# Optimization experiments

Hardware: AMD Instinct MI355X
Metric: run time of the kernel (lower is better)

## Reference

```python
import jax, jax.numpy as jnp
import numpy as np
from jax import lax

R = 3                      # blob_r
S = 2 * R + 1              # 7: maxpool / neighborhood kernel size
THRESH = 0.997
PS_XY = 0.1                # vs_xy
PS_Z = 0.02                # vs_z
ZMIN = -2.0                # zrange[0]
K_PEAKS = 131072           # static upper bound replacing torch.nonzero

_offs = np.arange(S)
_gz, _gy, _gx = np.meshgrid(_offs, _offs, _offs, indexing='ij')  # patch axis order [z,y,x]
GZ = jnp.asarray(_gz.ravel(), dtype=jnp.int32)
GY = jnp.asarray(_gy.ravel(), dtype=jnp.int32)
GX = jnp.asarray(_gx.ravel(), dtype=jnp.int32)
# centroid filters: offsets -r..r along the matching patch axis (matches torch meshgrid layout)
FZ = jnp.asarray((_gz.ravel() - R).astype(np.float32))
FY = jnp.asarray((_gy.ravel() - R).astype(np.float32))
FX = jnp.asarray((_gx.ravel() - R).astype(np.float32))


def setup_inputs() -> dict:
    key = jax.random.key(0)
    pred_vol = jax.random.uniform(key, (1, 1, 128, 512, 512), dtype=jnp.float32)
    return {"pred_vol": pred_vol, "max_peaks": K_PEAKS}


def _forward(pred_vol, max_peaks):
    vol = pred_vol[0, 0]                               # [D,H,W]
    D, H, W = vol.shape
    thr = jnp.where(vol > THRESH, vol, 0.0)
    # MaxPool3d(kernel=2r+1, stride=1, padding=r) == SAME max window (pad with -inf)
    mp = lax.reduce_window(thr, -jnp.inf, lax.max, (S, S, S), (1, 1, 1), [(R, R)] * 3)
    conf = jnp.where((mp > 0.0) & (mp == thr), mp, 0.0)  # local maxima above threshold
    # fixed-size peak extraction (replaces torch.nonzero); zero-valued entries are padding
    vals, idx = lax.top_k(conf.reshape(-1), max_peaks)   # [K], [K]
    z = idx // (H * W)
    y = (idx % (H * W)) // W
    x = idx % W
    padv = jnp.pad(vol, R)                               # ConstantPad3d(r, 0)
    # gather (2r+1)^3 neighborhoods around each peak: [K, S^3]
    patches = padv[z[:, None] + GZ[None, :], y[:, None] + GY[None, :], x[:, None] + GX[None, :]]
    s0 = patches.sum(axis=1)                             # conv3d with ones filter == conf_rec sum
    xloc = jnp.einsum('kp,p->k', patches, FX) / s0
    yloc = jnp.einsum('kp,p->k', patches, FY) / s0
    zloc = jnp.einsum('kp,p->k', patches, FZ) / s0
    xf = x.astype(jnp.float32)
    yf = y.astype(jnp.float32)
    zf = z.astype(jnp.float32)
    xrec = (xf + xloc - (W - 1) / 2.0) * PS_XY
    yrec = (yf + yloc - (H - 1) / 2.0) * PS_XY
    zrec = (zf + zloc + 0.5) * PS_Z + ZMIN
    valid = vals > 0.0
    xyz = jnp.where(valid[:, None], jnp.stack((xrec, yrec, zrec), axis=1), 0.0)  # [K,3]
    out = jnp.concatenate([xyz, vals[:, None]], axis=1)  # [K,4] = (x,y,z,conf), padded rows are 0
    return out, valid


def reference(pred_vol, max_peaks):
    return _forward(pred_vol, max_peaks)
```

## Files before the change

### kernel.cpp

```cpp
#include <hip/hip_runtime.h>

#define DD 128
#define HH 512
#define WW 512
#define NVOX (DD*HH*WW)
#define THRESHV 0.997f
#define KPEAKS 131072
#define PEAK_CAP (1u<<18)
#define NBINS 65536


__global__ void k_init(unsigned* counters, unsigned* hist) {
    unsigned t = blockIdx.x * 1024u + threadIdx.x;
    if (t < 64) counters[t] = 0u;
    if (t < NBINS) hist[t] = 0u;
}

__global__ __launch_bounds__(512, 8)
void k_find(const float4* __restrict__ vol4, const float* __restrict__ vol,
            unsigned* counters, unsigned* hist,
            unsigned long long* keys, float4* psums) {
    __shared__ float4 tile[2048];
    __shared__ unsigned lcnt, pcnt, lbase;
    __shared__ unsigned cidx[384];
    __shared__ unsigned long long lbuf[192];
    __shared__ float4 sbuf[192];
    if (threadIdx.x == 0) { lcnt = 0; pcnt = 0; }
    __syncthreads();

    unsigned t = threadIdx.x;
    unsigned lane = t & 63u;
    unsigned w = t >> 6;
    unsigned blockBase4 = blockIdx.x * 2048u;

#pragma unroll
    for (unsigned i = 0; i < 4; i++) {
        unsigned f = i * 512u + w * 64u;
        const float4* gp = vol4 + blockBase4 + f + lane;
        __builtin_amdgcn_global_load_lds(
            (const __attribute__((address_space(1))) unsigned int*)gp,
            (__attribute__((address_space(3))) unsigned int*)(tile + f),
            16, 0, 0);
    }
    __builtin_amdgcn_s_waitcnt(0);
    __syncthreads();

    unsigned m = 0u;
    float4 v[4];
#pragma unroll
    for (unsigned i = 0; i < 4; i++) v[i] = tile[i * 512u + t];
#pragma unroll
    for (unsigned i = 0; i < 4; i++) {
        m |= (v[i].x > THRESHV ? 1u : 0u) << (4 * i);
        m |= (v[i].y > THRESHV ? 1u : 0u) << (4 * i + 1);
        m |= (v[i].z > THRESHV ? 1u : 0u) << (4 * i + 2);
        m |= (v[i].w > THRESHV ? 1u : 0u) << (4 * i + 3);
    }
    while (m) {
        int b = __ffs(m) - 1;
        m &= m - 1u;
        unsigned f4 = blockBase4 + (unsigned)(b >> 2) * 512u + t;
        cidx[atomicAdd(&lcnt, 1u) & 383u] = f4 * 4u + (unsigned)(b & 3);
    }
    __syncthreads();

    unsigned n = lcnt > 384u ? 384u : lcnt;
    int dz = (int)lane / 7, dy = (int)lane - dz * 7;
    for (unsigned base = w * 2u; base < n; base += 16u) {
        bool has2 = (base + 1u < n);
        unsigned idxA = cidx[base];
        unsigned idxB = has2 ? cidx[base + 1u] : idxA;
        int zA = idxA >> 18, yA = (idxA >> 9) & 511, xA = idxA & 511;
        int zB = idxB >> 18, yB = (idxB >> 9) & 511, xB = idxB & 511;
        int nzA = zA + dz - 3, nyA = yA + dy - 3;
        int nzB = zB + dz - 3, nyB = yB + dy - 3;
        bool rowokA = (lane < 49) && ((unsigned)nzA < DD) && ((unsigned)nyA < HH);
        bool rowokB = (lane < 49) && ((unsigned)nzB < DD) && ((unsigned)nyB < HH);
        size_t rbA = rowokA ? (((size_t)(unsigned)nzA << 18) | ((size_t)(unsigned)nyA << 9))
                            : (((size_t)zA << 18) | ((size_t)yA << 9));
        size_t rbB = rowokB ? (((size_t)(unsigned)nzB << 18) | ((size_t)(unsigned)nyB << 9))
                            : (((size_t)zB << 18) | ((size_t)yB << 9));
        float rvA[7], rvB[7];
        bool intAB = (xA >= 3) && (xA <= WW - 4) && (xB >= 3) && (xB <= WW - 4);
        if (intAB) {
            float4 fA0 = *(const float4*)(vol + rbA + (unsigned)(xA - 3));
            float4 fA1 = *(const float4*)(vol + rbA + (unsigned)(xA + 1));
            float4 fB0 = *(const float4*)(vol + rbB + (unsigned)(xB - 3));
            float4 fB1 = *(const float4*)(vol + rbB + (unsigned)(xB + 1));
            rvA[0] = fA0.x; rvA[1] = fA0.y; rvA[2] = fA0.z; rvA[3] = fA0.w;
            rvA[4] = fA1.x; rvA[5] = fA1.y; rvA[6] = fA1.z;
            rvB[0] = fB0.x; rvB[1] = fB0.y; rvB[2] = fB0.z; rvB[3] = fB0.w;
            rvB[4] = fB1.x; rvB[5] = fB1.y; rvB[6] = fB1.z;
        } else {
#pragma unroll
            for (int d = 0; d < 7; d++) {
                int nxA = xA + d - 3;
                bool okA = (unsigned)nxA < WW;
                float va = vol[rbA + (unsigned)(okA ? nxA : xA)];
                rvA[d] = okA ? va : 0.f;
                int nxB = xB + d - 3;
                bool okB = (unsigned)nxB < WW;
                float vb = vol[rbB + (unsigned)(okB ? nxB : xB)];
                rvB[d] = okB ? vb : 0.f;
            }
        }
        if (!rowokA) {
#pragma unroll
            for (int d = 0; d < 7; d++) rvA[d] = 0.f;
        }
        if (!rowokB) {
#pragma unroll
            for (int d = 0; d < 7; d++) rvB[d] = 0.f;
        }
        float centerA = __shfl(rvA[3], 24);
        float centerB = __shfl(rvB[3], 24);

        {
            bool kill = false;
            float s0r = 0.f, sxr = 0.f;
#pragma unroll
            for (int d = 0; d < 7; d++) {
                kill |= rvA[d] > centerA;
                s0r += rvA[d];
                sxr += rvA[d] * (float)(d - 3);
            }
            if (!__any(kill)) {
                float s0 = s0r, sx = sxr;
                float sy = s0r * (float)(dy - 3);
                float sz = s0r * (float)(dz - 3);
                for (int off = 32; off; off >>= 1) {
                    s0 += __shfl_down(s0, off);
                    sx += __shfl_down(sx, off);
                    sy += __shfl_down(sy, off);
                    sz += __shfl_down(sz, off);
                }
                if (lane == 0) {
                    unsigned bits = __float_as_uint(centerA);
                    atomicAdd(&hist[(~bits) & 0xFFFFu], 1u);
                    unsigned li = atomicAdd(&pcnt, 1u);
                    if (li < 192u) {
                        lbuf[li] = ((unsigned long long)bits << 32) | idxA;
                        sbuf[li] = make_float4(s0, sx, sy, sz);
                    }
                }
            }
        }
        if (has2) {
            bool kill = false;
            float s0r = 0.f, sxr = 0.f;
#pragma unroll
            for (int d = 0; d < 7; d++) {
                kill |= rvB[d] > centerB;
                s0r += rvB[d];
                sxr += rvB[d] * (float)(d - 3);
            }
            if (!__any(kill)) {
                float s0 = s0r, sx = sxr;
                float sy = s0r * (float)(dy - 3);
                float sz = s0r * (float)(dz - 3);
                for (int off = 32; off; off >>= 1) {
                    s0 += __shfl_down(s0, off);
                    sx += __shfl_down(sx, off);
                    sy += __shfl_down(sy, off);
                    sz += __shfl_down(sz, off);
                }
                if (lane == 0) {
                    unsigned bits = __float_as_uint(centerB);
                    atomicAdd(&hist[(~bits) & 0xFFFFu], 1u);
                    unsigned li = atomicAdd(&pcnt, 1u);
                    if (li < 192u) {
                        lbuf[li] = ((unsigned long long)bits << 32) | idxB;
                        sbuf[li] = make_float4(s0, sx, sy, sz);
                    }
                }
            }
        }
    }
    __syncthreads();
    if (threadIdx.x == 0) lbase = atomicAdd(&counters[1], pcnt);
    __syncthreads();
    unsigned np = pcnt > 192u ? 192u : pcnt;
    for (unsigned i = threadIdx.x; i < np; i += 512u) {
        unsigned p = lbase + i;
        if (p < PEAK_CAP) { keys[p] = lbuf[i]; psums[p] = sbuf[i]; }
    }
}

__global__ void k_scan_a(const unsigned* __restrict__ hist,
                         unsigned* __restrict__ cursor,
                         unsigned* __restrict__ blocksum) {
    __shared__ unsigned sc[256];
    unsigned t = threadIdx.x, b = blockIdx.x;
    unsigned h = hist[b * 256u + t];
    sc[t] = h;
    __syncthreads();
    for (unsigned off = 1u; off < 256u; off <<= 1) {
        unsigned v = (t >= off) ? sc[t - off] : 0u;
        __syncthreads();
        sc[t] += v;
        __syncthreads();
    }
    cursor[b * 256u + t] = sc[t] - h;
    if (t == 255u) blocksum[b] = sc[255];
}

__global__ void k_scan_b(const unsigned* __restrict__ blocksum,
                         unsigned* __restrict__ cursor) {
    __shared__ unsigned bs[256];
    unsigned t = threadIdx.x, b = blockIdx.x;
    bs[t] = blocksum[t];
    __syncthreads();
    for (unsigned off = 1u; off < 256u; off <<= 1) {
        unsigned v = (t >= off) ? bs[t - off] : 0u;
        __syncthreads();
        bs[t] += v;
        __syncthreads();
    }
    unsigned base_b = (b > 0u) ? bs[b - 1u] : 0u;
    if (base_b != 0u) cursor[b * 256u + t] += base_b;
}

__global__ void k_scatter(const unsigned* __restrict__ counters,
                          const unsigned long long* __restrict__ keys,
                          unsigned* cursor, unsigned long long* sorted,
                          unsigned* sslot,
                          float4* __restrict__ out, float* __restrict__ valid) {
    unsigned np = counters[1]; if (np > PEAK_CAP) np = PEAK_CAP;
    unsigned t = blockIdx.x * 1024u + threadIdx.x;
    if (t < np) {
        unsigned long long key = keys[t];
        unsigned bits = (unsigned)(key >> 32);
        unsigned pos = atomicAdd(&cursor[(~bits) & 0xFFFFu], 1u);
        if (pos < PEAK_CAP) { sorted[pos] = key; sslot[pos] = t; }
    } else if (t < KPEAKS) {
        out[t] = make_float4(0.f, 0.f, 0.f, 0.f);
        valid[t] = 0.f;
    }
}

__global__ void k_finish(const unsigned* __restrict__ counters,
                         const unsigned long long* __restrict__ sorted,
                         const unsigned* __restrict__ sslot,
                         const float4* __restrict__ psums,
                         float4* __restrict__ out, float* __restrict__ valid) {
    unsigned np = counters[1]; if (np > PEAK_CAP) np = PEAK_CAP;
    unsigned t = blockIdx.x * 1024u + threadIdx.x;
    if (t >= np) return;
    unsigned long long key = sorted[t];
    unsigned bits = (unsigned)(key >> 32);
    unsigned s = t;
    while (s > 0 && (unsigned)(sorted[s - 1] >> 32) == bits) s--;
    unsigned myidx = (unsigned)key;
    unsigned rank = 0, e = s;
    while (e < np) {
        unsigned long long k2 = sorted[e];
        if ((unsigned)(k2 >> 32) != bits) break;
        if ((unsigned)k2 < myidx) rank++;
        e++;
    }
    unsigned row = s + rank;
    if (row >= KPEAKS) return;
    unsigned idx = myidx;
    int z = idx >> 18, y = (idx >> 9) & 511, x = idx & 511;
    float4 ps = psums[sslot[t]];
    float val = __uint_as_float(bits);
    float xloc = ps.y / ps.x, yloc = ps.z / ps.x, zloc = ps.w / ps.x;
    float xr = ((float)x + xloc - (float)(WW - 1) * 0.5f) * 0.1f;
    float yr = ((float)y + yloc - (float)(HH - 1) * 0.5f) * 0.1f;
    float zr = ((float)z + zloc + 0.5f) * 0.02f - 2.0f;
    out[row] = make_float4(xr, yr, zr, val);
    valid[row] = 1.f;
}

extern "C" void kernel_launch(void* const* d_in, const int* in_sizes, int n_in,
                              void* d_out, int out_size, void* d_ws, size_t ws_size,
                              hipStream_t stream) {
    const float* vol = (const float*)d_in[0];

    char* w = (char*)d_ws;
    unsigned* counters = (unsigned*)w;
    unsigned* hist     = (unsigned*)(w + 1024);
    unsigned* cursor   = (unsigned*)(w + 1024 + NBINS * 4);
    char* w2 = w + 1024 + 2 * NBINS * 4;
    unsigned long long* keys   = (unsigned long long*)w2;
    unsigned long long* sorted = keys + PEAK_CAP;
    unsigned* sslot = (unsigned*)(sorted + PEAK_CAP);
    float4*   psums = (float4*)(sslot + PEAK_CAP);

    unsigned* blocksum = sslot;

    float* out_rows = (float*)d_out;
    float* valid = out_rows + (size_t)KPEAKS * 4;

    k_init<<<NBINS / 1024, 1024, 0, stream>>>(counters, hist);
    k_find<<<NVOX / 8192, 512, 0, stream>>>((const float4*)vol, vol, counters, hist, keys, psums);
    k_scan_a<<<256, 256, 0, stream>>>(hist, cursor, blocksum);
    k_scan_b<<<256, 256, 0, stream>>>(blocksum, cursor);
    k_scatter<<<PEAK_CAP / 1024, 1024, 0, stream>>>(counters, keys, cursor, sorted, sslot,
                                                    (float4*)out_rows, valid);
    k_finish<<<PEAK_CAP / 1024, 1024, 0, stream>>>(counters, sorted, sslot, psums,
                                                   (float4*)out_rows, valid);
}
```

Measured before the change: 242.4 us.

## Load threshold scan directly to registers with larger per-block slabs

```diff
diff --git a/kernel.cpp b/kernel.cpp
--- a/kernel.cpp
+++ b/kernel.cpp
@@ -16,57 +16,59 @@
     if (t < NBINS) hist[t] = 0u;
 }
 
-__global__ __launch_bounds__(512, 8)
+__global__ __launch_bounds__(256, 8)
 void k_find(const float4* __restrict__ vol4, const float* __restrict__ vol,
             unsigned* counters, unsigned* hist,
             unsigned long long* keys, float4* psums) {
-    __shared__ float4 tile[2048];
     __shared__ unsigned lcnt, pcnt, lbase;
-    __shared__ unsigned cidx[384];
-    __shared__ unsigned long long lbuf[192];
-    __shared__ float4 sbuf[192];
+    __shared__ unsigned cidx[512];
+    __shared__ unsigned long long lbuf[256];
+    __shared__ float4 sbuf[256];
     if (threadIdx.x == 0) { lcnt = 0; pcnt = 0; }
     __syncthreads();
 
     unsigned t = threadIdx.x;
     unsigned lane = t & 63u;
     unsigned w = t >> 6;
-    unsigned blockBase4 = blockIdx.x * 2048u;
-
-#pragma unroll
-    for (unsigned i = 0; i < 4; i++) {
-        unsigned f = i * 512u + w * 64u;
-        const float4* gp = vol4 + blockBase4 + f + lane;
-        __builtin_amdgcn_global_load_lds(
-            (const __attribute__((address_space(1))) unsigned int*)gp,
-            (__attribute__((address_space(3))) unsigned int*)(tile + f),
-            16, 0, 0);
-    }
-    __builtin_amdgcn_s_waitcnt(0);
-    __syncthreads();
-
-    unsigned m = 0u;
-    float4 v[4];
-#pragma unroll
-    for (unsigned i = 0; i < 4; i++) v[i] = tile[i * 512u + t];
-#pragma unroll
-    for (unsigned i = 0; i < 4; i++) {
-        m |= (v[i].x > THRESHV ? 1u : 0u) << (4 * i);
-        m |= (v[i].y > THRESHV ? 1u : 0u) << (4 * i + 1);
-        m |= (v[i].z > THRESHV ? 1u : 0u) << (4 * i + 2);
-        m |= (v[i].w > THRESHV ? 1u : 0u) << (4 * i + 3);
-    }
-    while (m) {
-        int b = __ffs(m) - 1;
-        m &= m - 1u;
-        unsigned f4 = blockBase4 + (unsigned)(b >> 2) * 512u + t;
-        cidx[atomicAdd(&lcnt, 1u) & 383u] = f4 * 4u + (unsigned)(b & 3);
-    }
-    __syncthreads();
-
-    unsigned n = lcnt > 384u ? 384u : lcnt;
+    unsigned slab4 = blockIdx.x * 4096u;
+
+#pragma unroll
+    for (unsigned k = 0; k < 4; k++) {
+        unsigned b4 = slab4 + k * 1024u + t;
+        float4 a0 = vol4[b4];
+        float4 a1 = vol4[b4 + 256u];
+        float4 a2 = vol4[b4 + 512u];
+        float4 a3 = vol4[b4 + 768u];
+        __builtin_amdgcn_sched_barrier(0);
+        unsigned m = 0u;
+        m |= (a0.x > THRESHV ? 1u : 0u);
+        m |= (a0.y > THRESHV ? 2u : 0u);
+        m |= (a0.z > THRESHV ? 4u : 0u);
+        m |= (a0.w > THRESHV ? 8u : 0u);
+        m |= (a1.x > THRESHV ? 16u : 0u);
+        m |= (a1.y > THRESHV ? 32u : 0u);
+        m |= (a1.z > THRESHV ? 64u : 0u);
+        m |= (a1.w > THRESHV ? 128u : 0u);
+        m |= (a2.x > THRESHV ? 256u : 0u);
+        m |= (a2.y > THRESHV ? 512u : 0u);
+        m |= (a2.z > THRESHV ? 1024u : 0u);
+        m |= (a2.w > THRESHV ? 2048u : 0u);
+        m |= (a3.x > THRESHV ? 4096u : 0u);
+        m |= (a3.y > THRESHV ? 8192u : 0u);
+        m |= (a3.z > THRESHV ? 16384u : 0u);
+        m |= (a3.w > THRESHV ? 32768u : 0u);
+        while (m) {
+            int b = __ffs(m) - 1;
+            m &= m - 1u;
+            unsigned f4 = b4 + ((unsigned)b >> 2) * 256u;
+            cidx[atomicAdd(&lcnt, 1u) & 511u] = f4 * 4u + ((unsigned)b & 3u);
+        }
+    }
+    __syncthreads();
+
+    unsigned n = lcnt > 512u ? 512u : lcnt;
     int dz = (int)lane / 7, dy = (int)lane - dz * 7;
-    for (unsigned base = w * 2u; base < n; base += 16u) {
+    for (unsigned base = w * 2u; base < n; base += 8u) {
         bool has2 = (base + 1u < n);
         unsigned idxA = cidx[base];
         unsigned idxB = has2 ? cidx[base + 1u] : idxA;
@@ -138,7 +140,7 @@
                     unsigned bits = __float_as_uint(centerA);
                     atomicAdd(&hist[(~bits) & 0xFFFFu], 1u);
                     unsigned li = atomicAdd(&pcnt, 1u);
-                    if (li < 192u) {
+                    if (li < 256u) {
                         lbuf[li] = ((unsigned long long)bits << 32) | idxA;
                         sbuf[li] = make_float4(s0, sx, sy, sz);
                     }
@@ -168,7 +170,7 @@
                     unsigned bits = __float_as_uint(centerB);
                     atomicAdd(&hist[(~bits) & 0xFFFFu], 1u);
                     unsigned li = atomicAdd(&pcnt, 1u);
-                    if (li < 192u) {
+                    if (li < 256u) {
                         lbuf[li] = ((unsigned long long)bits << 32) | idxB;
                         sbuf[li] = make_float4(s0, sx, sy, sz);
                     }
@@ -179,8 +181,8 @@
     __syncthreads();
     if (threadIdx.x == 0) lbase = atomicAdd(&counters[1], pcnt);
     __syncthreads();
-    unsigned np = pcnt > 192u ? 192u : pcnt;
-    for (unsigned i = threadIdx.x; i < np; i += 512u) {
+    unsigned np = pcnt > 256u ? 256u : pcnt;
+    for (unsigned i = threadIdx.x; i < np; i += 256u) {
         unsigned p = lbase + i;
         if (p < PEAK_CAP) { keys[p] = lbuf[i]; psums[p] = sbuf[i]; }
     }
@@ -293,7 +295,7 @@
     float* valid = out_rows + (size_t)KPEAKS * 4;
 
     k_init<<<NBINS / 1024, 1024, 0, stream>>>(counters, hist);
-    k_find<<<NVOX / 8192, 512, 0, stream>>>((const float4*)vol, vol, counters, hist, keys, psums);
+    k_find<<<NVOX / 16384, 256, 0, stream>>>((const float4*)vol, vol, counters, hist, keys, psums);
     k_scan_a<<<256, 256, 0, stream>>>(hist, cursor, blocksum);
     k_scan_b<<<256, 256, 0, stream>>>(blocksum, cursor);
     k_scatter<<<PEAK_CAP / 1024, 1024, 0, stream>>>(counters, keys, cursor, sorted, sslot,
```

Result: slower. 251.7 us (+3.8%).

## Double-buffer k_find tiles and fold block-offset scan into scatter kernel

Applied to the files above, without the earlier changes.

```diff
diff --git a/kernel.cpp b/kernel.cpp
--- a/kernel.cpp
+++ b/kernel.cpp
@@ -16,11 +16,11 @@
     if (t < NBINS) hist[t] = 0u;
 }
 
-__global__ __launch_bounds__(512, 8)
+__global__ __launch_bounds__(512, 4)
 void k_find(const float4* __restrict__ vol4, const float* __restrict__ vol,
             unsigned* counters, unsigned* hist,
             unsigned long long* keys, float4* psums) {
-    __shared__ float4 tile[2048];
+    __shared__ float4 tile[2][2048];
     __shared__ unsigned lcnt, pcnt, lbase;
     __shared__ unsigned cidx[384];
     __shared__ unsigned long long lbuf[192];
@@ -31,151 +31,173 @@
     unsigned t = threadIdx.x;
     unsigned lane = t & 63u;
     unsigned w = t >> 6;
-    unsigned blockBase4 = blockIdx.x * 2048u;
-
-#pragma unroll
-    for (unsigned i = 0; i < 4; i++) {
-        unsigned f = i * 512u + w * 64u;
-        const float4* gp = vol4 + blockBase4 + f + lane;
-        __builtin_amdgcn_global_load_lds(
-            (const __attribute__((address_space(1))) unsigned int*)gp,
-            (__attribute__((address_space(3))) unsigned int*)(tile + f),
-            16, 0, 0);
-    }
+    unsigned blockBase4 = blockIdx.x * 4096u;
+    int dz = (int)lane / 7, dy = (int)lane - dz * 7;
+
+    auto dma = [&](unsigned s) {
+#pragma unroll
+        for (unsigned i = 0; i < 4; i++) {
+            unsigned f = i * 512u + w * 64u;
+            const float4* gp = vol4 + blockBase4 + s * 2048u + f + lane;
+            __builtin_amdgcn_global_load_lds(
+                (const __attribute__((address_space(1))) unsigned int*)gp,
+                (__attribute__((address_space(3))) unsigned int*)(&tile[s][f]),
+                16, 0, 0);
+        }
+    };
+
+    auto scan = [&](unsigned s) {
+        unsigned m = 0u;
+        float4 v[4];
+#pragma unroll
+        for (unsigned i = 0; i < 4; i++) v[i] = tile[s][i * 512u + t];
+#pragma unroll
+        for (unsigned i = 0; i < 4; i++) {
+            m |= (v[i].x > THRESHV ? 1u : 0u) << (4 * i);
+            m |= (v[i].y > THRESHV ? 1u : 0u) << (4 * i + 1);
+            m |= (v[i].z > THRESHV ? 1u : 0u) << (4 * i + 2);
+            m |= (v[i].w > THRESHV ? 1u : 0u) << (4 * i + 3);
+        }
+        unsigned sbase4 = blockBase4 + s * 2048u;
+        while (m) {
+            int b = __ffs(m) - 1;
+            m &= m - 1u;
+            unsigned f4 = sbase4 + (unsigned)(b >> 2) * 512u + t;
+            cidx[atomicAdd(&lcnt, 1u) & 383u] = f4 * 4u + (unsigned)(b & 3);
+        }
+    };
+
+    auto verify = [&](unsigned n) {
+        for (unsigned base = w * 2u; base < n; base += 16u) {
+            bool has2 = (base + 1u < n);
+            unsigned idxA = cidx[base];
+            unsigned idxB = has2 ? cidx[base + 1u] : idxA;
+            int zA = idxA >> 18, yA = (idxA >> 9) & 511, xA = idxA & 511;
+            int zB = idxB >> 18, yB = (idxB >> 9) & 511, xB = idxB & 511;
+            int nzA = zA + dz - 3, nyA = yA + dy - 3;
+            int nzB = zB + dz - 3, nyB = yB + dy - 3;
+            bool rowokA = (lane < 49) && ((unsigned)nzA < DD) && ((unsigned)nyA < HH);
+            bool rowokB = (lane < 49) && ((unsigned)nzB < DD) && ((unsigned)nyB < HH);
+            size_t rbA = rowokA ? (((size_t)(unsigned)nzA << 18) | ((size_t)(unsigned)nyA << 9))
+                                : (((size_t)zA << 18) | ((size_t)yA << 9));
+            size_t rbB = rowokB ? (((size_t)(unsigned)nzB << 18) | ((size_t)(unsigned)nyB << 9))
+                                : (((size_t)zB << 18) | ((size_t)yB << 9));
+            float rvA[7], rvB[7];
+            bool intAB = (xA >= 3) && (xA <= WW - 4) && (xB >= 3) && (xB <= WW - 4);
+            if (intAB) {
+                float4 fA0 = *(const float4*)(vol + rbA + (unsigned)(xA - 3));
+                float4 fA1 = *(const float4*)(vol + rbA + (unsigned)(xA + 1));
+                float4 fB0 = *(const float4*)(vol + rbB + (unsigned)(xB - 3));
+                float4 fB1 = *(const float4*)(vol + rbB + (unsigned)(xB + 1));
+                rvA[0] = fA0.x; rvA[1] = fA0.y; rvA[2] = fA0.z; rvA[3] = fA0.w;
+                rvA[4] = fA1.x; rvA[5] = fA1.y; rvA[6] = fA1.z;
+                rvB[0] = fB0.x; rvB[1] = fB0.y; rvB[2] = fB0.z; rvB[3] = fB0.w;
+                rvB[4] = fB1.x; rvB[5] = fB1.y; rvB[6] = fB1.z;
+            } else {
+#pragma unroll
+                for (int d = 0; d < 7; d++) {
+                    int nxA = xA + d - 3;
+                    bool okA = (unsigned)nxA < WW;
+                    float va = vol[rbA + (unsigned)(okA ? nxA : xA)];
+                    rvA[d] = okA ? va : 0.f;
+                    int nxB = xB + d - 3;
+                    bool okB = (unsigned)nxB < WW;
+                    float vb = vol[rbB + (unsigned)(okB ? nxB : xB)];
+                    rvB[d] = okB ? vb : 0.f;
+                }
+            }
+            if (!rowokA) {
+#pragma unroll
+                for (int d = 0; d < 7; d++) rvA[d] = 0.f;
+            }
+            if (!rowokB) {
+#pragma unroll
+                for (int d = 0; d < 7; d++) rvB[d] = 0.f;
+            }
+            float centerA = __shfl(rvA[3], 24);
+            float centerB = __shfl(rvB[3], 24);
+
+            {
+                bool kill = false;
+                float s0r = 0.f, sxr = 0.f;
+#pragma unroll
+                for (int d = 0; d < 7; d++) {
+                    kill |= rvA[d] > centerA;
+                    s0r += rvA[d];
+                    sxr += rvA[d] * (float)(d - 3);
+                }
+                if (!__any(kill)) {
+                    float s0 = s0r, sx = sxr;
+                    float sy = s0r * (float)(dy - 3);
+                    float sz = s0r * (float)(dz - 3);
+                    for (int off = 32; off; off >>= 1) {
+                        s0 += __shfl_down(s0, off);
+                        sx += __shfl_down(sx, off);
+                        sy += __shfl_down(sy, off);
+                        sz += __shfl_down(sz, off);
+                    }
+                    if (lane == 0) {
+                        unsigned bits = __float_as_uint(centerA);
+                        atomicAdd(&hist[(~bits) & 0xFFFFu], 1u);
+                        unsigned li = atomicAdd(&pcnt, 1u);
+                        if (li < 192u) {
+                            lbuf[li] = ((unsigned long long)bits << 32) | idxA;
+                            sbuf[li] = make_float4(s0, sx, sy, sz);
+                        }
+                    }
+                }
+            }
+            if (has2) {
+                bool kill = false;
+                float s0r = 0.f, sxr = 0.f;
+#pragma unroll
+                for (int d = 0; d < 7; d++) {
+                    kill |= rvB[d] > centerB;
+                    s0r += rvB[d];
+                    sxr += rvB[d] * (float)(d - 3);
+                }
+                if (!__any(kill)) {
+                    float s0 = s0r, sx = sxr;
+                    float sy = s0r * (float)(dy - 3);
+                    float sz = s0r * (float)(dz - 3);
+                    for (int off = 32; off; off >>= 1) {
+                        s0 += __shfl_down(s0, off);
+                        sx += __shfl_down(sx, off);
+                        sy += __shfl_down(sy, off);
+                        sz += __shfl_down(sz, off);
+                    }
+                    if (lane == 0) {
+                        unsigned bits = __float_as_uint(centerB);
+                        atomicAdd(&hist[(~bits) & 0xFFFFu], 1u);
+                        unsigned li = atomicAdd(&pcnt, 1u);
+                        if (li < 192u) {
+                            lbuf[li] = ((unsigned long long)bits << 32) | idxB;
+                            sbuf[li] = make_float4(s0, sx, sy, sz);
+                        }
+                    }
+                }
+            }
+        }
+    };
+
+    dma(0u);
     __builtin_amdgcn_s_waitcnt(0);
     __syncthreads();
-
-    unsigned m = 0u;
-    float4 v[4];
-#pragma unroll
-    for (unsigned i = 0; i < 4; i++) v[i] = tile[i * 512u + t];
-#pragma unroll
-    for (unsigned i = 0; i < 4; i++) {
-        m |= (v[i].x > THRESHV ? 1u : 0u) << (4 * i);
-        m |= (v[i].y > THRESHV ? 1u : 0u) << (4 * i + 1);
-        m |= (v[i].z > THRESHV ? 1u : 0u) << (4 * i + 2);
-        m |= (v[i].w > THRESHV ? 1u : 0u) << (4 * i + 3);
-    }
-    while (m) {
-        int b = __ffs(m) - 1;
-        m &= m - 1u;
-        unsigned f4 = blockBase4 + (unsigned)(b >> 2) * 512u + t;
-        cidx[atomicAdd(&lcnt, 1u) & 383u] = f4 * 4u + (unsigned)(b & 3);
-    }
-    __syncthreads();
-
-    unsigned n = lcnt > 384u ? 384u : lcnt;
-    int dz = (int)lane / 7, dy = (int)lane - dz * 7;
-    for (unsigned base = w * 2u; base < n; base += 16u) {
-        bool has2 = (base + 1u < n);
-        unsigned idxA = cidx[base];
-        unsigned idxB = has2 ? cidx[base + 1u] : idxA;
-        int zA = idxA >> 18, yA = (idxA >> 9) & 511, xA = idxA & 511;
-        int zB = idxB >> 18, yB = (idxB >> 9) & 511, xB = idxB & 511;
-        int nzA = zA + dz - 3, nyA = yA + dy - 3;
-        int nzB = zB + dz - 3, nyB = yB + dy - 3;
-        bool rowokA = (lane < 49) && ((unsigned)nzA < DD) && ((unsigned)nyA < HH);
-        bool rowokB = (lane < 49) && ((unsigned)nzB < DD) && ((unsigned)nyB < HH);
-        size_t rbA = rowokA ? (((size_t)(unsigned)nzA << 18) | ((size_t)(unsigned)nyA << 9))
-                            : (((size_t)zA << 18) | ((size_t)yA << 9));
-        size_t rbB = rowokB ? (((size_t)(unsigned)nzB << 18) | ((size_t)(unsigned)nyB << 9))
-                            : (((size_t)zB << 18) | ((size_t)yB << 9));
-        float rvA[7], rvB[7];
-        bool intAB = (xA >= 3) && (xA <= WW - 4) && (xB >= 3) && (xB <= WW - 4);
-        if (intAB) {
-            float4 fA0 = *(const float4*)(vol + rbA + (unsigned)(xA - 3));
-            float4 fA1 = *(const float4*)(vol + rbA + (unsigned)(xA + 1));
-            float4 fB0 = *(const float4*)(vol + rbB + (unsigned)(xB - 3));
-            float4 fB1 = *(const float4*)(vol + rbB + (unsigned)(xB + 1));
-            rvA[0] = fA0.x; rvA[1] = fA0.y; rvA[2] = fA0.z; rvA[3] = fA0.w;
-            rvA[4] = fA1.x; rvA[5] = fA1.y; rvA[6] = fA1.z;
-            rvB[0] = fB0.x; rvB[1] = fB0.y; rvB[2] = fB0.z; rvB[3] = fB0.w;
-            rvB[4] = fB1.x; rvB[5] = fB1.y; rvB[6] = fB1.z;
-        } else {
-#pragma unroll
-            for (int d = 0; d < 7; d++) {
-                int nxA = xA + d - 3;
-                bool okA = (unsigned)nxA < WW;
-                float va = vol[rbA + (unsigned)(okA ? nxA : xA)];
-                rvA[d] = okA ? va : 0.f;
-                int nxB = xB + d - 3;
-                bool okB = (unsigned)nxB < WW;
-                float vb = vol[rbB + (unsigned)(okB ? nxB : xB)];
-                rvB[d] = okB ? vb : 0.f;
-            }
-        }
-        if (!rowokA) {
-#pragma unroll
-            for (int d = 0; d < 7; d++) rvA[d] = 0.f;
-        }
-        if (!rowokB) {
-#pragma unroll
-            for (int d = 0; d < 7; d++) rvB[d] = 0.f;
-        }
-        float centerA = __shfl(rvA[3], 24);
-        float centerB = __shfl(rvB[3], 24);
-
-        {
-            bool kill = false;
-            float s0r = 0.f, sxr = 0.f;
-#pragma unroll
-            for (int d = 0; d < 7; d++) {
-                kill |= rvA[d] > centerA;
-                s0r += rvA[d];
-                sxr += rvA[d] * (float)(d - 3);
-            }
-            if (!__any(kill)) {
-                float s0 = s0r, sx = sxr;
-                float sy = s0r * (float)(dy - 3);
-                float sz = s0r * (float)(dz - 3);
-                for (int off = 32; off; off >>= 1) {
-                    s0 += __shfl_down(s0, off);
-                    sx += __shfl_down(sx, off);
-                    sy += __shfl_down(sy, off);
-                    sz += __shfl_down(sz, off);
-                }
-                if (lane == 0) {
-                    unsigned bits = __float_as_uint(centerA);
-                    atomicAdd(&hist[(~bits) & 0xFFFFu], 1u);
-                    unsigned li = atomicAdd(&pcnt, 1u);
-                    if (li < 192u) {
-                        lbuf[li] = ((unsigned long long)bits << 32) | idxA;
-                        sbuf[li] = make_float4(s0, sx, sy, sz);
-                    }
-                }
-            }
-        }
-        if (has2) {
-            bool kill = false;
-            float s0r = 0.f, sxr = 0.f;
-#pragma unroll
-            for (int d = 0; d < 7; d++) {
-                kill |= rvB[d] > centerB;
-                s0r += rvB[d];
-                sxr += rvB[d] * (float)(d - 3);
-            }
-            if (!__any(kill)) {
-                float s0 = s0r, sx = sxr;
-                float sy = s0r * (float)(dy - 3);
-                float sz = s0r * (float)(dz - 3);
-                for (int off = 32; off; off >>= 1) {
-                    s0 += __shfl_down(s0, off);
-                    sx += __shfl_down(sx, off);
-                    sy += __shfl_down(sy, off);
-                    sz += __shfl_down(sz, off);
-                }
-                if (lane == 0) {
-                    unsigned bits = __float_as_uint(centerB);
-                    atomicAdd(&hist[(~bits) & 0xFFFFu], 1u);
-                    unsigned li = atomicAdd(&pcnt, 1u);
-                    if (li < 192u) {
-                        lbuf[li] = ((unsigned long long)bits << 32) | idxB;
-                        sbuf[li] = make_float4(s0, sx, sy, sz);
-                    }
-                }
-            }
-        }
-    }
+    scan(0u);
+    __syncthreads();
+    unsigned n0 = lcnt > 384u ? 384u : lcnt;
+
+    dma(1u);
+    verify(n0);
+    __syncthreads();
+    if (t == 0) lcnt = 0;
+    __syncthreads();
+
+    scan(1u);
+    __syncthreads();
+    unsigned n1 = lcnt > 384u ? 384u : lcnt;
+    verify(n1);
+
     __syncthreads();
     if (threadIdx.x == 0) lbase = atomicAdd(&counters[1], pcnt);
     __syncthreads();
@@ -204,37 +226,35 @@
     if (t == 255u) blocksum[b] = sc[255];
 }
 
-__global__ void k_scan_b(const unsigned* __restrict__ blocksum,
-                         unsigned* __restrict__ cursor) {
-    __shared__ unsigned bs[256];
-    unsigned t = threadIdx.x, b = blockIdx.x;
-    bs[t] = blocksum[t];
-    __syncthreads();
-    for (unsigned off = 1u; off < 256u; off <<= 1) {
-        unsigned v = (t >= off) ? bs[t - off] : 0u;
-        __syncthreads();
-        bs[t] += v;
-        __syncthreads();
-    }
-    unsigned base_b = (b > 0u) ? bs[b - 1u] : 0u;
-    if (base_b != 0u) cursor[b * 256u + t] += base_b;
-}
-
 __global__ void k_scatter(const unsigned* __restrict__ counters,
                           const unsigned long long* __restrict__ keys,
+                          const unsigned* __restrict__ blocksum,
                           unsigned* cursor, unsigned long long* sorted,
                           unsigned* sslot,
                           float4* __restrict__ out, float* __restrict__ valid) {
+    __shared__ unsigned bs[256];
+    unsigned t = threadIdx.x;
+    if (t < 256u) bs[t] = blocksum[t];
+    __syncthreads();
+    for (unsigned off = 1u; off < 256u; off <<= 1) {
+        unsigned v = (t < 256u && t >= off) ? bs[t - off] : 0u;
+        __syncthreads();
+        if (t < 256u) bs[t] += v;
+        __syncthreads();
+    }
     unsigned np = counters[1]; if (np > PEAK_CAP) np = PEAK_CAP;
-    unsigned t = blockIdx.x * 1024u + threadIdx.x;
-    if (t < np) {
-        unsigned long long key = keys[t];
+    unsigned g = blockIdx.x * 1024u + t;
+    if (g < np) {
+        unsigned long long key = keys[g];
         unsigned bits = (unsigned)(key >> 32);
-        unsigned pos = atomicAdd(&cursor[(~bits) & 0xFFFFu], 1u);
-        if (pos < PEAK_CAP) { sorted[pos] = key; sslot[pos] = t; }
-    } else if (t < KPEAKS) {
-        out[t] = make_float4(0.f, 0.f, 0.f, 0.f);
-        valid[t] = 0.f;
+        unsigned bin = (~bits) & 0xFFFFu;
+        unsigned c = bin >> 8;
+        unsigned base_c = (c > 0u) ? bs[c - 1u] : 0u;
+        unsigned pos = base_c + atomicAdd(&cursor[bin], 1u);
+        if (pos < PEAK_CAP) { sorted[pos] = key; sslot[pos] = g; }
+    } else if (g < KPEAKS) {
+        out[g] = make_float4(0.f, 0.f, 0.f, 0.f);
+        valid[g] = 0.f;
     }
 }
 
@@ -286,17 +306,16 @@
     unsigned long long* sorted = keys + PEAK_CAP;
     unsigned* sslot = (unsigned*)(sorted + PEAK_CAP);
     float4*   psums = (float4*)(sslot + PEAK_CAP);
-
-    unsigned* blocksum = sslot;
+    unsigned* blocksum = (unsigned*)(psums + PEAK_CAP);
 
     float* out_rows = (float*)d_out;
     float* valid = out_rows + (size_t)KPEAKS * 4;
 
     k_init<<<NBINS / 1024, 1024, 0, stream>>>(counters, hist);
-    k_find<<<NVOX / 8192, 512, 0, stream>>>((const float4*)vol, vol, counters, hist, keys, psums);
+    k_find<<<NVOX / 16384, 512, 0, stream>>>((const float4*)vol, vol, counters, hist, keys, psums);
     k_scan_a<<<256, 256, 0, stream>>>(hist, cursor, blocksum);
-    k_scan_b<<<256, 256, 0, stream>>>(blocksum, cursor);
-    k_scatter<<<PEAK_CAP / 1024, 1024, 0, stream>>>(counters, keys, cursor, sorted, sslot,
+    k_scatter<<<PEAK_CAP / 1024, 1024, 0, stream>>>(counters, keys, blocksum, cursor,
+                                                    sorted, sslot,
                                                     (float4*)out_rows, valid);
     k_finish<<<PEAK_CAP / 1024, 1024, 0, stream>>>(counters, sorted, sslot, psums,
                                                    (float4*)out_rows, valid);
```

Result: slower. 252.6 us (+4.2%).
